# Performance work log

Hardware: AMD Instinct MI355X
Metric: run time of the kernel (lower is better)

Reference implementation:

```python
import jax, jax.numpy as jnp
import numpy as np

B, S, D_IN, D_OUT = 4, 2048, 1024, 1024

def setup_inputs() -> dict:
    key = jax.random.key(0)
    kx, kq, kk, kv = jax.random.split(key, 4)
    x = jax.random.normal(kx, (B, S, D_IN), dtype=jnp.float32)
    # torch nn.Linear weight is [d_out, d_in]; we store the transposed [d_in, d_out]
    # so y = x @ W, scaled like default init to keep magnitudes sane.
    scale = 1.0 / np.sqrt(D_IN)
    Wq = jax.random.normal(kq, (D_IN, D_OUT), dtype=jnp.float32) * scale
    Wk = jax.random.normal(kk, (D_IN, D_OUT), dtype=jnp.float32) * scale
    Wv = jax.random.normal(kv, (D_IN, D_OUT), dtype=jnp.float32) * scale
    return {"x": x, "Wq": Wq, "Wk": Wk, "Wv": Wv}

def reference(x, Wq, Wk, Wv):
    b, n, _ = x.shape
    q = jnp.einsum('bnd,de->bne', x, Wq)   # [B,S,D_OUT]
    k = jnp.einsum('bnd,de->bne', x, Wk)
    v = jnp.einsum('bnd,de->bne', x, Wv)
    scores = jnp.einsum('bqe,bke->bqk', q, k) / jnp.sqrt(jnp.float32(k.shape[-1]))
    causal = jnp.triu(jnp.ones((n, n), dtype=bool), k=1)  # True above diagonal -> masked
    scores = jnp.where(causal[None, :, :], -jnp.inf, scores)
    weights = jax.nn.softmax(scores, axis=-1)
    # dropout p=0.0 (deterministic baseline) -> identity
    context = jnp.einsum('bqk,bke->bqe', weights, v)
    return context
```

## Files before the change

kernel.cpp:

```cpp
#include <hip/hip_runtime.h>
#include <hip/hip_bf16.h>

#define BB 4
#define SS 2048
#define DD 1024

typedef __attribute__((ext_vector_type(8))) short bf16x8;
typedef __attribute__((ext_vector_type(4))) float f32x4;

__device__ __forceinline__ ushort f2bf(float f) {
  unsigned u = __float_as_uint(f);
  unsigned r = (u + 0x7fffu + ((u >> 16) & 1u)) >> 16;
  return (ushort)r;
}

__device__ __forceinline__ void gload_lds16(const void* g, void* l) {
  __builtin_amdgcn_global_load_lds(
      (const __attribute__((address_space(1))) void*)g,
      (__attribute__((address_space(3))) void*)l, 16, 0, 0);
}

__global__ __launch_bounds__(256) void cast_x_kernel(const float* __restrict__ x,
                                                     ushort* __restrict__ xb) {
  const int i = blockIdx.x * 256 + threadIdx.x;
#pragma unroll
  for (int j = 0; j < 4; j++) {
    const int idx = i + j * 524288;
    const float4 a = ((const float4*)x)[idx];
    ushort4 o;
    o.x = f2bf(a.x); o.y = f2bf(a.y); o.z = f2bf(a.z); o.w = f2bf(a.w);
    ((ushort4*)xb)[idx] = o;
  }
}

__global__ __launch_bounds__(256) void cast_transpose_w(const float* __restrict__ W0,
                                                        const float* __restrict__ W1,
                                                        const float* __restrict__ W2,
                                                        ushort* __restrict__ Wt) {
  const float* W = blockIdx.z == 0 ? W0 : (blockIdx.z == 1 ? W1 : W2);
  ushort* O = Wt + (size_t)blockIdx.z * DD * DD;
  __shared__ ushort t[32][33];
  const int n0 = blockIdx.x * 32, k0 = blockIdx.y * 32;
  const int tx = threadIdx.x, ty = threadIdx.y;
#pragma unroll
  for (int j = 0; j < 4; j++) {
    int k = k0 + ty + j * 8;
    t[ty + j * 8][tx] = f2bf(W[(size_t)k * DD + n0 + tx]);
  }
  __syncthreads();
#pragma unroll
  for (int j = 0; j < 4; j++) {
    int n = ty + j * 8;
    O[(size_t)(n0 + n) * DD + k0 + tx] = t[tx][n];
  }
}

template <int BM, int BN, int GMODE, bool EXPMASK, bool OUT_BF16>
__global__ __launch_bounds__(512) void gemm8(const ushort* __restrict__ A, int lda, size_t strA,
                                             const ushort* __restrict__ Bt, int ldb, size_t strB,
                                             void* __restrict__ C, int ldc, size_t strC, int K,
                                             int NBX) {
  constexpr int LA = BM / 64;
  constexpr int LB = BN / 64;
  constexpr int FM = BM / 32;
  constexpr int FN = BN / 64;
  int nb, mb, bz;
  if (GMODE == 2) {
    constexpr int T = 136;
    int flat = blockIdx.x + T * blockIdx.z;
    flat = (flat & 7) * ((T * BB) >> 3) + (flat >> 3);
    bz = flat / T;
    int i = flat % T;
    mb = (int)((sqrtf(8.f * i + 1.f) - 1.f) * 0.5f);
    while ((mb + 1) * (mb + 2) / 2 <= i) ++mb;
    while (mb * (mb + 1) / 2 > i) --mb;
    nb = i - mb * (mb + 1) / 2;
  } else {
    const int nwg = gridDim.x;
    int L = (blockIdx.x & 7) * (nwg >> 3) + (blockIdx.x >> 3);
    nb = L % NBX;
    mb = L / NBX;
    bz = 0;
  }
  const ushort* Ab = A + (size_t)bz * strA;
  const ushort* Bb = Bt + (size_t)bz * strB;

  __shared__ ushort lds[2][(BM + BN) * 64];

  const int tid = threadIdx.x;
  const int lane = tid & 63;
  const int wid = tid >> 6;
  const int wr = wid >> 2, wc = wid & 3;
  const int fr = lane & 15, qq = lane >> 4;
  const int sx = (fr & 7) << 4;

  const int NT = K >> 6;

  auto stage = [&](int kt, int buf) {
    ushort* As = &lds[buf][0];
    ushort* Bs = &lds[buf][BM * 64];
    const ushort* ga = Ab + (size_t)mb * BM * lda + kt * 64;
    const ushort* gb = Bb + (size_t)nb * BN * ldb + kt * 64;
#pragma unroll
    for (int j = 0; j < LA; j++) {
      int D = (j * 512 + tid) * 16;
      int r = D >> 7;
      int cb = (D & 127) ^ ((r & 7) << 4);
      gload_lds16(ga + (size_t)r * lda + (cb >> 1), (char*)As + D);
    }
#pragma unroll
    for (int j = 0; j < LB; j++) {
      int D = (j * 512 + tid) * 16;
      int r = D >> 7;
      int cb = (D & 127) ^ ((r & 7) << 4);
      gload_lds16(gb + (size_t)r * ldb + (cb >> 1), (char*)Bs + D);
    }
  };

  stage(0, 0);
  if (NT > 1) stage(1, 1);

  f32x4 acc[FM][FN] = {};

  for (int kt = 0; kt < NT; ++kt) {
    const int cur = kt & 1;
    if (kt < NT - 1) {
      if constexpr (LA + LB == 4) asm volatile("s_waitcnt vmcnt(4)" ::: "memory");
      else asm volatile("s_waitcnt vmcnt(0)" ::: "memory");
    } else {
      asm volatile("s_waitcnt vmcnt(0)" ::: "memory");
    }
    __builtin_amdgcn_s_barrier();
    __builtin_amdgcn_sched_barrier(0);

    const char* As = (const char*)&lds[cur][0];
    const char* Bs = (const char*)&lds[cur][BM * 64];
    __builtin_amdgcn_s_setprio(1);
#pragma unroll
    for (int ks = 0; ks < 2; ++ks) {
      const int kb = ks * 64 + qq * 16;
      bf16x8 a[FM], b[FN];
#pragma unroll
      for (int i = 0; i < FM; i++) {
        int r = wr * (BM / 2) + i * 16 + fr;
        a[i] = *(const bf16x8*)(As + r * 128 + (kb ^ sx));
      }
#pragma unroll
      for (int j = 0; j < FN; j++) {
        int r = wc * (BN / 4) + j * 16 + fr;
        b[j] = *(const bf16x8*)(Bs + r * 128 + (kb ^ sx));
      }
#pragma unroll
      for (int i = 0; i < FM; i++)
#pragma unroll
        for (int j = 0; j < FN; j++)
          acc[i][j] = __builtin_amdgcn_mfma_f32_16x16x32_bf16(a[i], b[j], acc[i][j], 0, 0, 0);
    }
    __builtin_amdgcn_s_setprio(0);
    __builtin_amdgcn_s_barrier();
    __builtin_amdgcn_sched_barrier(0);
    if (kt + 2 < NT) stage(kt + 2, cur);
  }

  const int col0 = nb * BN + wc * (BN / 4) + fr;
  const int row00 = mb * BM + wr * (BM / 2) + qq * 4;
  if (OUT_BF16) {
    ushort* Cb = (ushort*)C + (size_t)bz * strC;
#pragma unroll
    for (int i = 0; i < FM; i++)
#pragma unroll
      for (int rr = 0; rr < 4; rr++) {
        const int row = row00 + i * 16 + rr;
        size_t ro = (size_t)row * ldc;
#pragma unroll
        for (int j = 0; j < FN; j++) {
          float v = acc[i][j][rr];
          if (EXPMASK) {
            v = __expf(v * 0.03125f);
            if (col0 + j * 16 > row) v = 0.f;
          }
          Cb[ro + col0 + j * 16] = f2bf(v);
        }
      }
  } else {
    float* Cb = (float*)C + (size_t)bz * strC;
#pragma unroll
    for (int i = 0; i < FM; i++)
#pragma unroll
      for (int rr = 0; rr < 4; rr++) {
        size_t ro = (size_t)(row00 + i * 16 + rr) * ldc;
#pragma unroll
        for (int j = 0; j < FN; j++) Cb[ro + col0 + j * 16] = acc[i][j][rr];
      }
  }
}

__global__ __launch_bounds__(512) void pv_dual(const ushort* __restrict__ P,
                                               const ushort* __restrict__ Vt,
                                               float* __restrict__ out) {
  const int f = blockIdx.x;
  const int xcd = f & 7, L = f >> 3;
  const int bz = xcd >> 1, chalf = xcd & 1;
  const int nd = L & 15, c = chalf * 4 + (L >> 4);

  __shared__ ushort lds[2][(128 + 64) * 64];
  __shared__ float lds_l[2][64];

  const int tid = threadIdx.x;
  const int lane = tid & 63, wid = tid >> 6;
  const int wr = wid >> 2, wc = wid & 3;
  const int fr = lane & 15, qq = lane >> 4;
  const int sx = (fr & 7) << 4;

  const ushort* Pb = P + (size_t)bz * SS * SS;
  const ushort* Bg = Vt + (size_t)bz * 2048 + (size_t)(nd * 64) * 8192;

  auto stageA = [&](int mb, int kt, int buf) {
    ushort* As = &lds[buf][0];
    const ushort* ga = Pb + (size_t)(mb * 128) * SS + kt * 64;
#pragma unroll
    for (int j = 0; j < 2; j++) {
      int D = (j * 512 + tid) * 16;
      int r = D >> 7;
      int cb = (D & 127) ^ ((r & 7) << 4);
      gload_lds16(ga + (size_t)r * SS + (cb >> 1), (char*)As + D);
    }
  };
  auto stageB = [&](int kt, int buf) {
    ushort* Bs = &lds[buf][128 * 64];
    const ushort* gb = Bg + kt * 64;
    int D = tid * 16;
    int r = D >> 7;
    int cb = (D & 127) ^ ((r & 7) << 4);
    gload_lds16(gb + (size_t)r * 8192 + (cb >> 1), (char*)Bs + D);
  };

#pragma unroll 1
  for (int ph = 0; ph < 2; ++ph) {
    const int mb = ph == 0 ? c : 15 - c;
    const int NT = 2 * (mb + 1);

    stageA(mb, 0, 0); stageB(0, 0);
    if (NT > 1) { stageA(mb, 1, 1); stageB(1, 1); }

    f32x4 acc[4] = {};
    float lsum[4] = {0.f, 0.f, 0.f, 0.f};

    for (int kt = 0; kt < NT; ++kt) {
      const int cur = kt & 1;
      if (kt < NT - 1) asm volatile("s_waitcnt vmcnt(3)" ::: "memory");
      else             asm volatile("s_waitcnt vmcnt(0)" ::: "memory");
      __builtin_amdgcn_s_barrier();
      __builtin_amdgcn_sched_barrier(0);

      const char* As = (const char*)&lds[cur][0];
      const char* Bs = (const char*)&lds[cur][128 * 64];
      __builtin_amdgcn_s_setprio(1);
#pragma unroll
      for (int ks = 0; ks < 2; ++ks) {
        const int kb = ks * 64 + qq * 16;
        bf16x8 a[4], b;
#pragma unroll
        for (int i = 0; i < 4; i++) {
          int r = wr * 64 + i * 16 + fr;
          a[i] = *(const bf16x8*)(As + r * 128 + (kb ^ sx));
        }
        b = *(const bf16x8*)(Bs + (wc * 16 + fr) * 128 + (kb ^ sx));
        if (wc == 0) {
#pragma unroll
          for (int i = 0; i < 4; i++)
#pragma unroll
            for (int e = 0; e < 8; e++)
              lsum[i] += __uint_as_float((unsigned)(unsigned short)a[i][e] << 16);
        }
#pragma unroll
        for (int i = 0; i < 4; i++)
          acc[i] = __builtin_amdgcn_mfma_f32_16x16x32_bf16(a[i], b, acc[i], 0, 0, 0);
      }
      __builtin_amdgcn_s_setprio(0);
      __builtin_amdgcn_s_barrier();
      __builtin_amdgcn_sched_barrier(0);
      if (kt + 2 < NT) { stageA(mb, kt + 2, cur); stageB(kt + 2, cur); }
    }

    if (wc == 0) {
#pragma unroll
      for (int i = 0; i < 4; i++) {
        lsum[i] += __shfl_xor(lsum[i], 16);
        lsum[i] += __shfl_xor(lsum[i], 32);
      }
      if (qq == 0) {
#pragma unroll
        for (int i = 0; i < 4; i++) lds_l[wr][i * 16 + fr] = lsum[i];
      }
    }
    __syncthreads();

    const int col = nd * 64 + wc * 16 + fr;
    const int row00 = mb * 128 + wr * 64 + qq * 4;
    float* ob = out + ((size_t)bz * SS) * DD;
#pragma unroll
    for (int i = 0; i < 4; i++)
#pragma unroll
      for (int rr = 0; rr < 4; rr++) {
        const float invl = 1.f / lds_l[wr][i * 16 + qq * 4 + rr];
        ob[(size_t)(row00 + i * 16 + rr) * DD + col] = acc[i][rr] * invl;
      }
    __syncthreads();
  }
}

extern "C" void kernel_launch(void* const* d_in, const int* in_sizes, int n_in,
                              void* d_out, int out_size, void* d_ws, size_t ws_size,
                              hipStream_t stream) {
  const float* x = (const float*)d_in[0];
  const float* Wq = (const float*)d_in[1];
  const float* Wk = (const float*)d_in[2];
  const float* Wv = (const float*)d_in[3];

  char* ws = (char*)d_ws;
  ushort* xb = (ushort*)(ws);
  ushort* Wt = (ushort*)(ws + 16777216);
  ushort* QK = (ushort*)(ws + 23068672);
  ushort* Vt = (ushort*)(ws + 56623104);
  ushort* P = (ushort*)(ws + 73400320);

  const size_t S2 = (size_t)SS * SS;
  const size_t SQ2 = (size_t)SS * 2048;

  cast_x_kernel<<<2048, 256, 0, stream>>>(x, xb);
  cast_transpose_w<<<dim3(DD / 32, DD / 32, 3), dim3(32, 8), 0, stream>>>(Wq, Wk, Wv, Wt);
  gemm8<128, 128, 1, false, true><<<dim3(1024), 512, 0, stream>>>(
      xb, DD, 0, Wt, DD, 0, QK, 2048, 0, DD, 16);
  gemm8<128, 128, 1, false, true><<<dim3(512), 512, 0, stream>>>(
      Wt + 2 * DD * DD, DD, 0, xb, DD, 0, Vt, BB * SS, 0, DD, 64);
  gemm8<128, 128, 2, true, true><<<dim3(136, 1, BB), 512, 0, stream>>>(
      QK, 2048, SQ2, QK + 1024, 2048, SQ2, P, SS, S2, DD, 0);
  pv_dual<<<dim3(512), 512, 0, stream>>>(P, Vt, (float*)d_out);

  (void)in_sizes; (void)n_in; (void)out_size; (void)ws_size;
}
```

Measured before the change: 159.6 us.

## Add 256x256 eight-phase pipelined GEMM for QK projection and MFMA row sums

The Q/K projection GEMM moves to a new 256x256-tile kernel. It splits each 64-wide K step into two halves with separate LDS buffers and interleaves global-to-LDS loads with MFMA phases under explicit barriers and waitcnts. The goal is more data reuse per tile and more load/compute overlap than the 128x128 gemm8. In pv_dual, the scalar per-element bf16 row-sum loop is replaced by an MFMA against a vector of ones, which removes the shuffle reduction. Risks are the larger tile halving the grid to 256 workgroups, higher register pressure from the 8x4 accumulators, and correctness of the new swizzle.

```diff
diff --git a/kernel.cpp b/kernel.cpp
--- a/kernel.cpp
+++ b/kernel.cpp
@@ -18,6 +18,11 @@
   __builtin_amdgcn_global_load_lds(
       (const __attribute__((address_space(1))) void*)g,
       (__attribute__((address_space(3))) void*)l, 16, 0, 0);
+}
+
+__device__ __forceinline__ void BARSB() {
+  __builtin_amdgcn_s_barrier();
+  __builtin_amdgcn_sched_barrier(0);
 }
 
 __global__ __launch_bounds__(256) void cast_x_kernel(const float* __restrict__ x,
@@ -55,15 +60,149 @@
   }
 }
 
-template <int BM, int BN, int GMODE, bool EXPMASK, bool OUT_BF16>
-__global__ __launch_bounds__(512) void gemm8(const ushort* __restrict__ A, int lda, size_t strA,
-                                             const ushort* __restrict__ Bt, int ldb, size_t strB,
+__global__ __launch_bounds__(512) void gemm256_8ph(const ushort* __restrict__ A, int lda,
+                                                   const ushort* __restrict__ Bt, int ldb,
+                                                   ushort* __restrict__ C, int ldc, int K,
+                                                   int NBCOLS) {
+  const int nwg = gridDim.x;
+  int ord = blockIdx.x;
+  int flat = (ord & 7) * (nwg >> 3) + (ord >> 3);
+  const int mb = flat / NBCOLS, nb = flat % NBCOLS;
+
+  __shared__ char ldsA[2][2][16384];
+  __shared__ char ldsB[2][2][16384];
+
+  const int tid = threadIdx.x;
+  const int lane = tid & 63, wid = tid >> 6;
+  const int wr = wid >> 2, wc = wid & 3;
+  const int fr = lane & 15, qq = lane >> 4;
+  const int kxor = ((qq ^ ((fr >> 1) & 3)) << 4);
+
+  const int srcE = (((tid & 3) ^ ((tid >> 3) & 3)) << 3);
+  const ushort* Ag_t = A + (size_t)(mb * 256 + (tid >> 2)) * lda + srcE;
+  const ushort* Bg_t = Bt + (size_t)(nb * 256 + (tid >> 2)) * ldb + srcE;
+
+  const int NT = K >> 6;
+
+  auto stA = [&](int buf, int kh, int kt) {
+#pragma unroll
+    for (int j = 0; j < 2; j++)
+      gload_lds16(Ag_t + (size_t)(j * 128) * lda + kt * 64 + kh * 32,
+                  &ldsA[buf][kh][(j * 512 + tid) * 16]);
+  };
+  auto stB = [&](int buf, int kh, int kt) {
+#pragma unroll
+    for (int j = 0; j < 2; j++)
+      gload_lds16(Bg_t + (size_t)(j * 128) * ldb + kt * 64 + kh * 32,
+                  &ldsB[buf][kh][(j * 512 + tid) * 16]);
+  };
+  auto ldA4 = [&](int buf, int kh, int mi0, bf16x8* o) {
+#pragma unroll
+    for (int i = 0; i < 4; i++)
+      o[i] = *(const bf16x8*)(&ldsA[buf][kh][0] +
+                              ((wr * 128 + (mi0 + i) * 16 + fr) << 6) + kxor);
+  };
+  auto ldB4 = [&](int buf, int kh, bf16x8* o) {
+#pragma unroll
+    for (int n = 0; n < 4; n++)
+      o[n] = *(const bf16x8*)(&ldsB[buf][kh][0] + ((wc * 64 + n * 16 + fr) << 6) + kxor);
+  };
+
+  f32x4 acc[8][4] = {};
+  bf16x8 a[4], b[4];
+
+#define MF16(MI0)                                                              \
+  do {                                                                         \
+    asm volatile("s_waitcnt lgkmcnt(0)" ::: "memory");                         \
+    __builtin_amdgcn_sched_barrier(0);                                         \
+    __builtin_amdgcn_s_setprio(1);                                             \
+    _Pragma("unroll") for (int i_ = 0; i_ < 4; i_++) {                         \
+      _Pragma("unroll") for (int n_ = 0; n_ < 4; n_++) {                       \
+        acc[(MI0) + i_][n_] = __builtin_amdgcn_mfma_f32_16x16x32_bf16(         \
+            a[i_], b[n_], acc[(MI0) + i_][n_], 0, 0, 0);                       \
+      }                                                                        \
+    }                                                                          \
+    __builtin_amdgcn_s_setprio(0);                                             \
+  } while (0)
+
+  stB(0, 0, 0); stA(0, 0, 0); stB(0, 1, 0); stA(0, 1, 0);
+  __builtin_amdgcn_sched_barrier(0);
+  asm volatile("s_waitcnt vmcnt(4)" ::: "memory");
+  stB(1, 0, 1); stA(1, 0, 1); stB(1, 1, 1);
+  __builtin_amdgcn_sched_barrier(0);
+  asm volatile("s_waitcnt vmcnt(6)" ::: "memory");
+  BARSB();
+
+  const int NIT = NT >> 1;
+  for (int it = 0; it < NIT; ++it) {
+    const int t = 2 * it;
+    const bool s2 = (t + 2 < NT), s3 = (t + 3 < NT);
+    ldA4(0, 0, 0, a); ldB4(0, 0, b);
+    stA(1, 1, t + 1);
+    BARSB();
+    MF16(0);
+    BARSB();
+    ldA4(0, 0, 4, a);
+    if (s2) stB(0, 0, t + 2);
+    BARSB();
+    MF16(4);
+    BARSB();
+    ldA4(0, 1, 0, a); ldB4(0, 1, b);
+    if (s2) stA(0, 0, t + 2);
+    BARSB();
+    MF16(0);
+    BARSB();
+    ldA4(0, 1, 4, a);
+    if (s2) stB(0, 1, t + 2);
+    BARSB();
+    MF16(4);
+    __builtin_amdgcn_sched_barrier(0);
+    if (s2) asm volatile("s_waitcnt vmcnt(6)" ::: "memory");
+    else    asm volatile("s_waitcnt vmcnt(0)" ::: "memory");
+    BARSB();
+    ldA4(1, 0, 0, a); ldB4(1, 0, b);
+    if (s2) stA(0, 1, t + 2);
+    BARSB();
+    MF16(0);
+    BARSB();
+    ldA4(1, 0, 4, a);
+    if (s3) stB(1, 0, t + 3);
+    BARSB();
+    MF16(4);
+    BARSB();
+    ldA4(1, 1, 0, a); ldB4(1, 1, b);
+    if (s3) stA(1, 0, t + 3);
+    BARSB();
+    MF16(0);
+    BARSB();
+    ldA4(1, 1, 4, a);
+    if (s3) stB(1, 1, t + 3);
+    BARSB();
+    MF16(4);
+    __builtin_amdgcn_sched_barrier(0);
+    if (s3) asm volatile("s_waitcnt vmcnt(6)" ::: "memory");
+    else    asm volatile("s_waitcnt vmcnt(0)" ::: "memory");
+    BARSB();
+  }
+#undef MF16
+
+  const int col0 = nb * 256 + wc * 64 + fr;
+  const int row00 = mb * 256 + wr * 128 + qq * 4;
+#pragma unroll
+  for (int i = 0; i < 8; i++)
+#pragma unroll
+    for (int rr = 0; rr < 4; rr++) {
+      size_t ro = (size_t)(row00 + i * 16 + rr) * ldc;
+#pragma unroll
+      for (int n = 0; n < 4; n++) C[ro + col0 + n * 16] = f2bf(acc[i][n][rr]);
+    }
+}
+
+template <int GMODE>
+__global__ __launch_bounds__(512) void gemm8(const ushort* __restrict__ A0, int lda, size_t strA,
+                                             const ushort* __restrict__ Bt0, int ldb, size_t strB,
                                              void* __restrict__ C, int ldc, size_t strC, int K,
                                              int NBX) {
-  constexpr int LA = BM / 64;
-  constexpr int LB = BN / 64;
-  constexpr int FM = BM / 32;
-  constexpr int FN = BN / 64;
   int nb, mb, bz;
   if (GMODE == 2) {
     constexpr int T = 136;
@@ -82,10 +221,10 @@
     mb = L / NBX;
     bz = 0;
   }
-  const ushort* Ab = A + (size_t)bz * strA;
-  const ushort* Bb = Bt + (size_t)bz * strB;
-
-  __shared__ ushort lds[2][(BM + BN) * 64];
+  const ushort* Ab = A0 + (size_t)bz * strA;
+  const ushort* Bb = Bt0 + (size_t)bz * strB;
+
+  __shared__ ushort lds[2][256 * 64];
 
   const int tid = threadIdx.x;
   const int lane = tid & 63;
@@ -98,18 +237,18 @@
 
   auto stage = [&](int kt, int buf) {
     ushort* As = &lds[buf][0];
-    ushort* Bs = &lds[buf][BM * 64];
-    const ushort* ga = Ab + (size_t)mb * BM * lda + kt * 64;
-    const ushort* gb = Bb + (size_t)nb * BN * ldb + kt * 64;
-#pragma unroll
-    for (int j = 0; j < LA; j++) {
+    ushort* Bs = &lds[buf][128 * 64];
+    const ushort* ga = Ab + (size_t)mb * 128 * lda + kt * 64;
+    const ushort* gb = Bb + (size_t)nb * 128 * ldb + kt * 64;
+#pragma unroll
+    for (int j = 0; j < 2; j++) {
       int D = (j * 512 + tid) * 16;
       int r = D >> 7;
       int cb = (D & 127) ^ ((r & 7) << 4);
       gload_lds16(ga + (size_t)r * lda + (cb >> 1), (char*)As + D);
     }
 #pragma unroll
-    for (int j = 0; j < LB; j++) {
+    for (int j = 0; j < 2; j++) {
       int D = (j * 512 + tid) * 16;
       int r = D >> 7;
       int cb = (D & 127) ^ ((r & 7) << 4);
@@ -120,40 +259,36 @@
   stage(0, 0);
   if (NT > 1) stage(1, 1);
 
-  f32x4 acc[FM][FN] = {};
+  f32x4 acc[4][2] = {};
 
   for (int kt = 0; kt < NT; ++kt) {
     const int cur = kt & 1;
-    if (kt < NT - 1) {
-      if constexpr (LA + LB == 4) asm volatile("s_waitcnt vmcnt(4)" ::: "memory");
-      else asm volatile("s_waitcnt vmcnt(0)" ::: "memory");
-    } else {
-      asm volatile("s_waitcnt vmcnt(0)" ::: "memory");
-    }
+    if (kt < NT - 1) asm volatile("s_waitcnt vmcnt(4)" ::: "memory");
+    else             asm volatile("s_waitcnt vmcnt(0)" ::: "memory");
     __builtin_amdgcn_s_barrier();
     __builtin_amdgcn_sched_barrier(0);
 
     const char* As = (const char*)&lds[cur][0];
-    const char* Bs = (const char*)&lds[cur][BM * 64];
+    const char* Bs = (const char*)&lds[cur][128 * 64];
     __builtin_amdgcn_s_setprio(1);
 #pragma unroll
     for (int ks = 0; ks < 2; ++ks) {
       const int kb = ks * 64 + qq * 16;
-      bf16x8 a[FM], b[FN];
-#pragma unroll
-      for (int i = 0; i < FM; i++) {
-        int r = wr * (BM / 2) + i * 16 + fr;
+      bf16x8 a[4], b[2];
+#pragma unroll
+      for (int i = 0; i < 4; i++) {
+        int r = wr * 64 + i * 16 + fr;
         a[i] = *(const bf16x8*)(As + r * 128 + (kb ^ sx));
       }
 #pragma unroll
-      for (int j = 0; j < FN; j++) {
-        int r = wc * (BN / 4) + j * 16 + fr;
+      for (int j = 0; j < 2; j++) {
+        int r = wc * 32 + j * 16 + fr;
         b[j] = *(const bf16x8*)(Bs + r * 128 + (kb ^ sx));
       }
 #pragma unroll
-      for (int i = 0; i < FM; i++)
-#pragma unroll
-        for (int j = 0; j < FN; j++)
+      for (int i = 0; i < 4; i++)
+#pragma unroll
+        for (int j = 0; j < 2; j++)
           acc[i][j] = __builtin_amdgcn_mfma_f32_16x16x32_bf16(a[i], b[j], acc[i][j], 0, 0, 0);
     }
     __builtin_amdgcn_s_setprio(0);
@@ -162,37 +297,25 @@
     if (kt + 2 < NT) stage(kt + 2, cur);
   }
 
-  const int col0 = nb * BN + wc * (BN / 4) + fr;
-  const int row00 = mb * BM + wr * (BM / 2) + qq * 4;
-  if (OUT_BF16) {
-    ushort* Cb = (ushort*)C + (size_t)bz * strC;
-#pragma unroll
-    for (int i = 0; i < FM; i++)
-#pragma unroll
-      for (int rr = 0; rr < 4; rr++) {
-        const int row = row00 + i * 16 + rr;
-        size_t ro = (size_t)row * ldc;
-#pragma unroll
-        for (int j = 0; j < FN; j++) {
-          float v = acc[i][j][rr];
-          if (EXPMASK) {
-            v = __expf(v * 0.03125f);
-            if (col0 + j * 16 > row) v = 0.f;
-          }
-          Cb[ro + col0 + j * 16] = f2bf(v);
+  const int col0 = nb * 128 + wc * 32 + fr;
+  const int row00 = mb * 128 + wr * 64 + qq * 4;
+  ushort* Cb = (ushort*)C + (size_t)bz * strC;
+#pragma unroll
+  for (int i = 0; i < 4; i++)
+#pragma unroll
+    for (int rr = 0; rr < 4; rr++) {
+      const int row = row00 + i * 16 + rr;
+      size_t ro = (size_t)row * ldc;
+#pragma unroll
+      for (int j = 0; j < 2; j++) {
+        float v = acc[i][j][rr];
+        if (GMODE == 2) {
+          v = __expf(v * 0.03125f);
+          if (col0 + j * 16 > row) v = 0.f;
         }
+        Cb[ro + col0 + j * 16] = f2bf(v);
       }
-  } else {
-    float* Cb = (float*)C + (size_t)bz * strC;
-#pragma unroll
-    for (int i = 0; i < FM; i++)
-#pragma unroll
-      for (int rr = 0; rr < 4; rr++) {
-        size_t ro = (size_t)(row00 + i * 16 + rr) * ldc;
-#pragma unroll
-        for (int j = 0; j < FN; j++) Cb[ro + col0 + j * 16] = acc[i][j][rr];
-      }
-  }
+    }
 }
 
 __global__ __launch_bounds__(512) void pv_dual(const ushort* __restrict__ P,
@@ -212,6 +335,10 @@
   const int fr = lane & 15, qq = lane >> 4;
   const int sx = (fr & 7) << 4;
 
+  bf16x8 ones;
+#pragma unroll
+  for (int e = 0; e < 8; e++) ones[e] = (short)0x3F80;
+
   const ushort* Pb = P + (size_t)bz * SS * SS;
   const ushort* Bg = Vt + (size_t)bz * 2048 + (size_t)(nd * 64) * 8192;
 
@@ -244,7 +371,7 @@
     if (NT > 1) { stageA(mb, 1, 1); stageB(1, 1); }
 
     f32x4 acc[4] = {};
-    float lsum[4] = {0.f, 0.f, 0.f, 0.f};
+    f32x4 accl[4] = {};
 
     for (int kt = 0; kt < NT; ++kt) {
       const int cur = kt & 1;
@@ -269,9 +396,7 @@
         if (wc == 0) {
 #pragma unroll
           for (int i = 0; i < 4; i++)
-#pragma unroll
-            for (int e = 0; e < 8; e++)
-              lsum[i] += __uint_as_float((unsigned)(unsigned short)a[i][e] << 16);
+            accl[i] = __builtin_amdgcn_mfma_f32_16x16x32_bf16(a[i], ones, accl[i], 0, 0, 0);
         }
 #pragma unroll
         for (int i = 0; i < 4; i++)
@@ -283,16 +408,11 @@
       if (kt + 2 < NT) { stageA(mb, kt + 2, cur); stageB(kt + 2, cur); }
     }
 
-    if (wc == 0) {
-#pragma unroll
-      for (int i = 0; i < 4; i++) {
-        lsum[i] += __shfl_xor(lsum[i], 16);
-        lsum[i] += __shfl_xor(lsum[i], 32);
-      }
-      if (qq == 0) {
-#pragma unroll
-        for (int i = 0; i < 4; i++) lds_l[wr][i * 16 + fr] = lsum[i];
-      }
+    if (wc == 0 && fr == 0) {
+#pragma unroll
+      for (int i = 0; i < 4; i++)
+#pragma unroll
+        for (int rr = 0; rr < 4; rr++) lds_l[wr][i * 16 + qq * 4 + rr] = accl[i][rr];
     }
     __syncthreads();
 
@@ -330,11 +450,10 @@
 
   cast_x_kernel<<<2048, 256, 0, stream>>>(x, xb);
   cast_transpose_w<<<dim3(DD / 32, DD / 32, 3), dim3(32, 8), 0, stream>>>(Wq, Wk, Wv, Wt);
-  gemm8<128, 128, 1, false, true><<<dim3(1024), 512, 0, stream>>>(
-      xb, DD, 0, Wt, DD, 0, QK, 2048, 0, DD, 16);
-  gemm8<128, 128, 1, false, true><<<dim3(512), 512, 0, stream>>>(
+  gemm8<1><<<dim3(512), 512, 0, stream>>>(
       Wt + 2 * DD * DD, DD, 0, xb, DD, 0, Vt, BB * SS, 0, DD, 64);
-  gemm8<128, 128, 2, true, true><<<dim3(136, 1, BB), 512, 0, stream>>>(
+  gemm256_8ph<<<dim3(256), 512, 0, stream>>>(xb, DD, Wt, DD, QK, 2048, DD, 8);
+  gemm8<2><<<dim3(136, 1, BB), 512, 0, stream>>>(
       QK, 2048, SQ2, QK + 1024, 2048, SQ2, P, SS, S2, DD, 0);
   pv_dual<<<dim3(512), 512, 0, stream>>>(P, Vt, (float*)d_out);
 
```

Result: faster. 152.6 us (-4.4%).
